# Performance work log

Measured on AMD Instinct MI355X. Metric: run time of the kernel, lower is better.

The kernel has to match this reference:

```python
import jax, jax.numpy as jnp
import numpy as np

N = 8192        # num nodes
E = 262144      # num edges (avg degree 32)
IN = 128        # in_features
OUT = 128       # out_features
ALPHA = 0.2     # LeakyReLU negative slope


def setup_inputs() -> dict:
    key = jax.random.key(0)
    k1, k2, k3, k4 = jax.random.split(key, 4)
    x = jax.random.normal(k1, (N, IN), dtype=jnp.float32)
    edge_index = jax.random.randint(k2, (2, E), 0, N, dtype=jnp.int32)
    W = jax.random.normal(k3, (IN, OUT), dtype=jnp.float32) * 0.05
    a = jax.random.normal(k4, (2 * OUT, 1), dtype=jnp.float32) * 0.05
    return {"x": x, "edge_index": edge_index, "W": W, "a": a}


def reference(x, edge_index, W, a):
    # Linear (no bias): Wh = x @ W  (W stored [in, out])
    Wh = x @ W                                   # [N, OUT]
    src, dst = edge_index[0], edge_index[1]      # [E], [E]
    # e = LeakyReLU([Wh_src || Wh_dst] @ a) computed without concat:
    a_src, a_dst = a[:OUT, 0], a[OUT:, 0]
    e = Wh[src] @ a_src + Wh[dst] @ a_dst        # [E]
    e = jnp.where(e > 0, e, ALPHA * e)           # LeakyReLU
    # Faithful to original: scatter into DENSE N x N, softmax full rows
    # (zeros at non-edge positions participate in the softmax).
    att = jnp.zeros((N, N), dtype=x.dtype).at[src, dst].set(e)
    att = jax.nn.softmax(att, axis=1)            # [N, N]
    # dropout p=0 in eval reference -> identity
    node_importance = att.sum(axis=0)            # [N]
    h_prime = att @ Wh                           # [N, OUT]
    return jax.nn.elu(h_prime), node_importance
```

## Files before the change

### kernel.cpp

```cpp
#include <hip/hip_runtime.h>
#include <math.h>

constexpr int N = 8192;
constexpr int E = 262144;
constexpr int CAP = 128;
constexpr int PAD = 16;

__device__ inline unsigned pack_bf16x2(float lo, float hi) {
    unsigned ul = __float_as_uint(lo);
    unsigned uh = __float_as_uint(hi);
    ul = ul + 0x7FFFu + ((ul >> 16) & 1u);
    uh = uh + 0x7FFFu + ((uh >> 16) & 1u);
    return (ul >> 16) | (uh & 0xFFFF0000u);
}

__global__ __launch_bounds__(256) void k1_kernel(
    const float* __restrict__ x, const float* __restrict__ W, const float* __restrict__ a,
    const int* __restrict__ ei,
    unsigned* __restrict__ Whb, float* __restrict__ s_src, float* __restrict__ s_dst,
    float* __restrict__ whcol, int* __restrict__ bucket, float* __restrict__ S_part) {
    int t = threadIdx.x, bid = blockIdx.x;
    if (bid < 512) {
        if (bid == 0 && t < 64) S_part[t * PAD] = 0.f;
        int i = bid * 256 + t;
        int2 us = ((const int2*)ei)[i];
        int2 vs = ((const int2*)(ei + E))[i];
        bucket[(size_t)us.x * CAP + (vs.x & (CAP - 1))] = vs.x + 1;
        bucket[(size_t)us.y * CAP + (vs.y & (CAP - 1))] = vs.y + 1;
    } else {
        __shared__ float spA[2][4], sqA[2][4];
        __shared__ float spB[2][4], sqB[2][4];
        __shared__ float wsum[2][128];
        int gb = bid - 512;
        int l = t & 63, w = t >> 6;
        int rg = w >> 1, ch = w & 1;
        int r0 = gb * 8 + rg * 4;
        int c = ch * 64 + l;
        int xbase = __builtin_amdgcn_readfirstlane(r0 * 128);
        const float* xb = x + xbase;
        float acc0 = 0.f, acc1 = 0.f, acc2 = 0.f, acc3 = 0.f;
        for (int kc = 0; kc < 128; kc += 16) {
            float4 xr[4][4];
#pragma unroll
            for (int r = 0; r < 4; r++)
#pragma unroll
                for (int j = 0; j < 4; j++)
                    xr[r][j] = *(const float4*)(xb + r * 128 + kc + j * 4);
#pragma unroll
            for (int j = 0; j < 16; j++) {
                float wv = W[(size_t)(kc + j) * 128 + c];
                float x0 = ((const float*)&xr[0][0])[j];
                float x1 = ((const float*)&xr[1][0])[j];
                float x2 = ((const float*)&xr[2][0])[j];
                float x3 = ((const float*)&xr[3][0])[j];
                acc0 += x0 * wv;
                acc1 += x1 * wv;
                acc2 += x2 * wv;
                acc3 += x3 * wv;
            }
        }
        float accs[4] = {acc0, acc1, acc2, acc3};
        wsum[rg][c] = acc0 + acc1 + acc2 + acc3;
#pragma unroll
        for (int r = 0; r < 4; r++) {
            float hi = __shfl_xor(accs[r], 1);
            if ((l & 1) == 0)
                Whb[(size_t)(r0 + r) * 64 + (c >> 1)] = pack_bf16x2(accs[r], hi);
        }
        float av = a[c], bv = a[128 + c];
#pragma unroll
        for (int r = 0; r < 4; r++) {
            float p = accs[r] * av, q = accs[r] * bv;
#pragma unroll
            for (int off = 32; off; off >>= 1) { p += __shfl_down(p, off); q += __shfl_down(q, off); }
            if (l == 0) {
                if (ch == 0) { spA[rg][r] = p; sqA[rg][r] = q; }
                else         { spB[rg][r] = p; sqB[rg][r] = q; }
            }
        }
        __syncthreads();
        if (t < 128) atomicAdd(&whcol[(gb & 7) * 128 + t], wsum[0][t] + wsum[1][t]);
        if (t < 8) {
            int rr = t & 3, grp = t >> 2;
            int row = gb * 8 + grp * 4 + rr;
            s_src[row] = spA[grp][rr] + spB[grp][rr];
            s_dst[row] = sqA[grp][rr] + sqB[grp][rr];
        }
    }
}

__global__ __launch_bounds__(256) void hprime_kernel(
    const unsigned* __restrict__ Whb, const float* __restrict__ whcol,
    const float* __restrict__ s_src, const float* __restrict__ s_dst,
    int* __restrict__ bucket, float* __restrict__ imp_acc,
    float* __restrict__ S_part, float* __restrict__ out) {
    __shared__ int cv[4][128];
    __shared__ float cw[4][128];
    __shared__ __align__(16) float cs[128];
    int t = threadIdx.x;
    if (t < 128) {
        float s = 0.f;
#pragma unroll
        for (int i = 0; i < 8; i++) s += whcol[i * 128 + t];
        cs[t] = s;
    }
    int wv = t >> 6, l = t & 63;
    int u = blockIdx.x * 4 + wv;
    size_t base = (size_t)u * CAP;
    int slot0 = bucket[base + l];
    int slot1 = bucket[base + 64 + l];
    bucket[base + l] = 0;
    bucket[base + 64 + l] = 0;
    int v0 = slot0 - 1, v1 = slot1 - 1;
    bool ok0 = (unsigned)v0 < (unsigned)N;
    bool ok1 = (unsigned)v1 < (unsigned)N;
    unsigned long long m0 = __ballot(ok0);
    unsigned long long m1 = __ballot(ok1);
    int c0 = __popcll(m0);
    int total = c0 + __popcll(m1);
    unsigned long long below = (1ull << l) - 1ull;
    if (ok0) cv[wv][__popcll(m0 & below)] = v0;
    if (ok1) cv[wv][c0 + __popcll(m1 & below)] = v1;
    __syncthreads();
    float ssrc = s_src[u];
    float contrib = 0.f;
    int myv = 0;
    float myw = 0.f;
    if (l < total) {
        myv = cv[wv][l];
        float e = ssrc + s_dst[myv];
        e = e > 0.f ? e : 0.2f * e;
        myw = expm1f(e);
        cw[wv][l] = myw;
        contrib = myw;
    }
    int myv2 = 0;
    float myw2 = 0.f;
    bool has2 = (l + 64) < total;
    if (has2) {
        myv2 = cv[wv][64 + l];
        float e2 = ssrc + s_dst[myv2];
        e2 = e2 > 0.f ? e2 : 0.2f * e2;
        myw2 = expm1f(e2);
        cw[wv][64 + l] = myw2;
        contrib += myw2;
    }
    __syncthreads();
#pragma unroll
    for (int off = 1; off < 64; off <<= 1) contrib += __shfl_xor(contrib, off);
    float inv = 1.f / (8192.f + contrib);
    if (l == 0) atomicAdd(&S_part[(u & 63) * PAD], inv);
    if (l < total) atomicAdd(&imp_acc[(size_t)myv * PAD], myw * inv);
    if (has2) atomicAdd(&imp_acc[(size_t)myv2 * PAD], myw2 * inv);

    int qw = l >> 4, ql = l & 15;
    float acc[8] = {0.f, 0.f, 0.f, 0.f, 0.f, 0.f, 0.f, 0.f};
    for (int j = 0; j < total; j += 4) {
        int jj = j + qw;
        int jr = jj < 127 ? jj : 127;
        bool ok = jj < total;
        int v = ok ? cv[wv][jr] : 0;
        float w = ok ? cw[wv][jr] : 0.f;
        uint4 tv = *(const uint4*)((const char*)Whb + (size_t)v * 256 + ql * 16);
        acc[0] += w * __uint_as_float(tv.x << 16);
        acc[1] += w * __uint_as_float(tv.x & 0xFFFF0000u);
        acc[2] += w * __uint_as_float(tv.y << 16);
        acc[3] += w * __uint_as_float(tv.y & 0xFFFF0000u);
        acc[4] += w * __uint_as_float(tv.z << 16);
        acc[5] += w * __uint_as_float(tv.z & 0xFFFF0000u);
        acc[6] += w * __uint_as_float(tv.w << 16);
        acc[7] += w * __uint_as_float(tv.w & 0xFFFF0000u);
    }
#pragma unroll
    for (int i = 0; i < 8; i++) {
        acc[i] += __shfl_down(acc[i], 32);
        acc[i] += __shfl_down(acc[i], 16);
    }
    if (qw == 0) {
        float4 cs0 = *(const float4*)&cs[ql * 8];
        float4 cs1 = *(const float4*)&cs[ql * 8 + 4];
        float h[8];
        h[0] = (cs0.x + acc[0]) * inv;
        h[1] = (cs0.y + acc[1]) * inv;
        h[2] = (cs0.z + acc[2]) * inv;
        h[3] = (cs0.w + acc[3]) * inv;
        h[4] = (cs1.x + acc[4]) * inv;
        h[5] = (cs1.y + acc[5]) * inv;
        h[6] = (cs1.z + acc[6]) * inv;
        h[7] = (cs1.w + acc[7]) * inv;
#pragma unroll
        for (int i = 0; i < 8; i++) h[i] = h[i] > 0.f ? h[i] : expm1f(h[i]);
        float* op = out + (size_t)u * 128 + ql * 8;
        *(float4*)op = make_float4(h[0], h[1], h[2], h[3]);
        *(float4*)(op + 4) = make_float4(h[4], h[5], h[6], h[7]);
    }
}

__global__ __launch_bounds__(256) void imp_kernel(
    const float* __restrict__ S_part, float* __restrict__ imp_acc,
    float* __restrict__ whcol, float* __restrict__ out) {
    __shared__ float sS[64];
    int t = threadIdx.x;
    if (t < 64) sS[t] = S_part[t * PAD];
    if (blockIdx.x == 31 && t < 128) {
#pragma unroll
        for (int i = 0; i < 8; i++) whcol[i * 128 + t] = 0.f;
    }
    __syncthreads();
    float S = 0.f;
#pragma unroll
    for (int i = 0; i < 64; i++) S += sS[i];
    int j = blockIdx.x * 256 + t;
    float v = imp_acc[(size_t)j * PAD];
    imp_acc[(size_t)j * PAD] = 0.f;
    out[(size_t)N * 128 + j] = S + v;
}

extern "C" void kernel_launch(void* const* d_in, const int* in_sizes, int n_in,
                              void* d_out, int out_size, void* d_ws, size_t ws_size,
                              hipStream_t stream) {
    const float* x = (const float*)d_in[0];
    const int* ei = (const int*)d_in[1];
    const float* W = (const float*)d_in[2];
    const float* a = (const float*)d_in[3];
    float* out = (float*)d_out;

    char* ws = (char*)d_ws;
    size_t o = 0;
    auto alloc = [&](size_t bytes) { char* p = ws + o; o += (bytes + 255) & ~(size_t)255; return p; };
    unsigned* Whb  = (unsigned*)alloc((size_t)N * 64 * 4);
    int* bucket    = (int*)alloc((size_t)N * CAP * 4);
    float* imp_acc = (float*)alloc((size_t)N * PAD * 4);
    float* whcol   = (float*)alloc(8 * 128 * 4);
    float* S_part  = (float*)alloc(64 * PAD * 4);
    float* s_src   = (float*)alloc(N * 4);
    float* s_dst   = (float*)alloc(N * 4);
    (void)ws_size;

    k1_kernel<<<dim3(1536), dim3(256), 0, stream>>>(x, W, a, ei, Whb, s_src, s_dst, whcol, bucket,
                                                    S_part);
    hprime_kernel<<<dim3(N / 4), dim3(256), 0, stream>>>(Whb, whcol, s_src, s_dst, bucket,
                                                         imp_acc, S_part, out);
    imp_kernel<<<dim3(32), dim3(256), 0, stream>>>(S_part, imp_acc, whcol, out);
}
```

Baseline: 101.7 us.

## Store Wh as FP8 e5m2 and fuse importance kernel via last-block counter

Wh is now stored as 8-bit e5m2 (the top byte of fp16) instead of bf16, which halves the bytes gathered per neighbour row in the attention-weighted aggregation. The separate importance-finalize kernel is removed: each hprime block bumps a global counter, and the last 32 blocks to arrive spin until every block has finished, then sum the S partials and write node_importance. This removes one kernel launch and halves the gather traffic. In exchange, Wh loses a lot of precision, which may break the accuracy tolerance. The spin-wait also assumes the finishing blocks can make forward progress.

```diff
diff --git a/kernel.cpp b/kernel.cpp
--- a/kernel.cpp
+++ b/kernel.cpp
@@ -5,23 +5,33 @@
 constexpr int E = 262144;
 constexpr int CAP = 128;
 constexpr int PAD = 16;
-
-__device__ inline unsigned pack_bf16x2(float lo, float hi) {
-    unsigned ul = __float_as_uint(lo);
-    unsigned uh = __float_as_uint(hi);
-    ul = ul + 0x7FFFu + ((ul >> 16) & 1u);
-    uh = uh + 0x7FFFu + ((uh >> 16) & 1u);
-    return (ul >> 16) | (uh & 0xFFFF0000u);
+constexpr int HP_BLOCKS = N / 4;
+constexpr int SLICES = 32;
+
+__device__ inline unsigned enc_e5m2(float f) {
+    union { _Float16 h; unsigned short u; } cv;
+    cv.h = (_Float16)f;
+    return (((unsigned)cv.u + 0x80u) >> 8) & 0xFFu;
+}
+
+__device__ inline float dec_f16(unsigned t) {
+    union { unsigned short u; _Float16 h; } cv;
+    cv.u = (unsigned short)t;
+    return (float)cv.h;
 }
 
 __global__ __launch_bounds__(256) void k1_kernel(
     const float* __restrict__ x, const float* __restrict__ W, const float* __restrict__ a,
     const int* __restrict__ ei,
     unsigned* __restrict__ Whb, float* __restrict__ s_src, float* __restrict__ s_dst,
-    float* __restrict__ whcol, int* __restrict__ bucket, float* __restrict__ S_part) {
+    float* __restrict__ whcol, int* __restrict__ bucket, float* __restrict__ S_part,
+    int* __restrict__ ctr) {
     int t = threadIdx.x, bid = blockIdx.x;
     if (bid < 512) {
-        if (bid == 0 && t < 64) S_part[t * PAD] = 0.f;
+        if (bid == 0) {
+            if (t < 64) S_part[t * PAD] = 0.f;
+            if (t == 64) *ctr = 0;
+        }
         int i = bid * 256 + t;
         int2 us = ((const int2*)ei)[i];
         int2 vs = ((const int2*)(ei + E))[i];
@@ -63,9 +73,11 @@
         wsum[rg][c] = acc0 + acc1 + acc2 + acc3;
 #pragma unroll
         for (int r = 0; r < 4; r++) {
-            float hi = __shfl_xor(accs[r], 1);
-            if ((l & 1) == 0)
-                Whb[(size_t)(r0 + r) * 64 + (c >> 1)] = pack_bf16x2(accs[r], hi);
+            unsigned b = enc_e5m2(accs[r]);
+            unsigned p = b | (((unsigned)__shfl_xor((int)b, 1)) << 8);
+            unsigned q = p | (((unsigned)__shfl_xor((int)p, 2)) << 16);
+            if ((l & 3) == 0)
+                Whb[(size_t)(r0 + r) * 32 + (c >> 2)] = q;
         }
         float av = a[c], bv = a[128 + c];
 #pragma unroll
@@ -90,13 +102,14 @@
 }
 
 __global__ __launch_bounds__(256) void hprime_kernel(
-    const unsigned* __restrict__ Whb, const float* __restrict__ whcol,
+    const unsigned* __restrict__ Whb, float* __restrict__ whcol,
     const float* __restrict__ s_src, const float* __restrict__ s_dst,
     int* __restrict__ bucket, float* __restrict__ imp_acc,
-    float* __restrict__ S_part, float* __restrict__ out) {
+    float* __restrict__ S_part, int* __restrict__ ctr, float* __restrict__ out) {
     __shared__ int cv[4][128];
     __shared__ float cw[4][128];
     __shared__ __align__(16) float cs[128];
+    __shared__ int rank_s;
     int t = threadIdx.x;
     if (t < 128) {
         float s = 0.f;
@@ -161,15 +174,15 @@
         bool ok = jj < total;
         int v = ok ? cv[wv][jr] : 0;
         float w = ok ? cw[wv][jr] : 0.f;
-        uint4 tv = *(const uint4*)((const char*)Whb + (size_t)v * 256 + ql * 16);
-        acc[0] += w * __uint_as_float(tv.x << 16);
-        acc[1] += w * __uint_as_float(tv.x & 0xFFFF0000u);
-        acc[2] += w * __uint_as_float(tv.y << 16);
-        acc[3] += w * __uint_as_float(tv.y & 0xFFFF0000u);
-        acc[4] += w * __uint_as_float(tv.z << 16);
-        acc[5] += w * __uint_as_float(tv.z & 0xFFFF0000u);
-        acc[6] += w * __uint_as_float(tv.w << 16);
-        acc[7] += w * __uint_as_float(tv.w & 0xFFFF0000u);
+        uint2 tv = *(const uint2*)((const char*)Whb + (size_t)v * 128 + ql * 8);
+        acc[0] += w * dec_f16(tv.x << 8);
+        acc[1] += w * dec_f16(tv.x);
+        acc[2] += w * dec_f16(tv.x >> 8);
+        acc[3] += w * dec_f16(tv.x >> 16);
+        acc[4] += w * dec_f16(tv.y << 8);
+        acc[5] += w * dec_f16(tv.y);
+        acc[6] += w * dec_f16(tv.y >> 8);
+        acc[7] += w * dec_f16(tv.y >> 16);
     }
 #pragma unroll
     for (int i = 0; i < 8; i++) {
@@ -194,25 +207,29 @@
         *(float4*)op = make_float4(h[0], h[1], h[2], h[3]);
         *(float4*)(op + 4) = make_float4(h[4], h[5], h[6], h[7]);
     }
-}
-
-__global__ __launch_bounds__(256) void imp_kernel(
-    const float* __restrict__ S_part, float* __restrict__ imp_acc,
-    float* __restrict__ whcol, float* __restrict__ out) {
-    __shared__ float sS[64];
-    int t = threadIdx.x;
-    if (t < 64) sS[t] = S_part[t * PAD];
-    if (blockIdx.x == 31 && t < 128) {
+
+    __threadfence();
+    __syncthreads();
+    if (t == 0) rank_s = atomicAdd(ctr, 1);
+    __syncthreads();
+    int slice = rank_s - (HP_BLOCKS - SLICES);
+    if ((unsigned)slice >= (unsigned)SLICES) return;
+    if (t == 0) {
+        while (atomicAdd(ctr, 0) < HP_BLOCKS) __builtin_amdgcn_s_sleep(2);
+    }
+    __syncthreads();
+    __threadfence();
+    if (t < 64) cs[t] = atomicAdd(&S_part[t * PAD], 0.f);
+    if (slice == SLICES - 1 && t < 128) {
 #pragma unroll
         for (int i = 0; i < 8; i++) whcol[i * 128 + t] = 0.f;
     }
     __syncthreads();
     float S = 0.f;
 #pragma unroll
-    for (int i = 0; i < 64; i++) S += sS[i];
-    int j = blockIdx.x * 256 + t;
-    float v = imp_acc[(size_t)j * PAD];
-    imp_acc[(size_t)j * PAD] = 0.f;
+    for (int i = 0; i < 64; i++) S += cs[i];
+    int j = slice * 256 + t;
+    float v = atomicExch(&imp_acc[(size_t)j * PAD], 0.f);
     out[(size_t)N * 128 + j] = S + v;
 }
 
@@ -228,18 +245,18 @@
     char* ws = (char*)d_ws;
     size_t o = 0;
     auto alloc = [&](size_t bytes) { char* p = ws + o; o += (bytes + 255) & ~(size_t)255; return p; };
-    unsigned* Whb  = (unsigned*)alloc((size_t)N * 64 * 4);
+    unsigned* Whb  = (unsigned*)alloc((size_t)N * 32 * 4);
     int* bucket    = (int*)alloc((size_t)N * CAP * 4);
     float* imp_acc = (float*)alloc((size_t)N * PAD * 4);
     float* whcol   = (float*)alloc(8 * 128 * 4);
     float* S_part  = (float*)alloc(64 * PAD * 4);
+    int* ctr       = (int*)alloc(256);
     float* s_src   = (float*)alloc(N * 4);
     float* s_dst   = (float*)alloc(N * 4);
     (void)ws_size;
 
     k1_kernel<<<dim3(1536), dim3(256), 0, stream>>>(x, W, a, ei, Whb, s_src, s_dst, whcol, bucket,
-                                                    S_part);
-    hprime_kernel<<<dim3(N / 4), dim3(256), 0, stream>>>(Whb, whcol, s_src, s_dst, bucket,
-                                                         imp_acc, S_part, out);
-    imp_kernel<<<dim3(32), dim3(256), 0, stream>>>(S_part, imp_acc, whcol, out);
-}
+                                                    S_part, ctr);
+    hprime_kernel<<<dim3(HP_BLOCKS), dim3(256), 0, stream>>>(Whb, whcol, s_src, s_dst, bucket,
+                                                             imp_acc, S_part, ctr, out);
+}
```

Result: slower. 268.8 us (+164.2%).
